# Kernel tuning notes

Hardware: AMD Instinct MI355X
Metric: run time of the kernel (lower is better)

Reference implementation:

```python
import jax, jax.numpy as jnp
import numpy as np

B, H, S, D = 2, 16, 2048, 128


def setup_inputs() -> dict:
    key = jax.random.key(0)
    kq, kk, kv = jax.random.split(key, 3)
    q = jax.random.normal(kq, (B, H, S, D), dtype=jnp.float32)
    k = jax.random.normal(kk, (B, H, S, D), dtype=jnp.float32)
    v = jax.random.normal(kv, (B, H, S, D), dtype=jnp.float32)
    scale = jnp.float32(1.0 / np.sqrt(D))
    return {"q": q, "k": k, "v": v, "scale": scale}


def reference(q, k, v, scale):
    # scores: [B, H, S, S]
    attn = jnp.einsum("bhqd,bhkd->bhqk", q, k) * scale
    attn = jnp.square(jax.nn.relu(attn))  # relu(x)^2 score function (no softmax)
    return jnp.einsum("bhqk,bhkd->bhqd", attn, v)
```

## Files before the change

kernel.cpp:

```cpp
#include <hip/hip_runtime.h>
#include <hip/hip_bf16.h>
#include <stdint.h>

#define S_LEN 2048
#define D_DIM 128
#define QT 128
#define KT 64
#define NT (S_LEN/KT)
#define TKT 32
#define TNT (S_LEN/TKT)

typedef float  f32x4  __attribute__((ext_vector_type(4)));
typedef float  f32x16 __attribute__((ext_vector_type(16)));
typedef short  bf16x8 __attribute__((ext_vector_type(8)));
typedef unsigned int uintx4 __attribute__((ext_vector_type(4)));

__device__ __forceinline__ short f2bf(float f) {
    return __builtin_bit_cast(short, __float2bfloat16(f));
}

__device__ __forceinline__ unsigned int pk2(float lo, float hi) {
    unsigned int d;
    asm("v_cvt_pk_bf16_f32 %0, %1, %2" : "=v"(d) : "v"(lo), "v"(hi));
    return d;
}

__device__ __forceinline__ void gload_lds16(const short* g, char* l) {
    __builtin_amdgcn_global_load_lds(
        (const __attribute__((address_space(1))) void*)g,
        (__attribute__((address_space(3))) void*)l,
        16, 0, 0);
}

__global__ __launch_bounds__(256)
void convert_k_kernel(const float* __restrict__ kin, short* __restrict__ kbf) {
    const size_t i = ((size_t)blockIdx.x * 256 + threadIdx.x) * 8;
    f32x4 a = *(const f32x4*)(kin + i);
    f32x4 c = *(const f32x4*)(kin + i + 4);
    bf16x8 t;
    t[0]=f2bf(a[0]); t[1]=f2bf(a[1]); t[2]=f2bf(a[2]); t[3]=f2bf(a[3]);
    t[4]=f2bf(c[0]); t[5]=f2bf(c[1]); t[6]=f2bf(c[2]); t[7]=f2bf(c[3]);
    *(bf16x8*)(kbf + i) = t;
}

__global__ __launch_bounds__(256)
void transpose_v_kernel(const float* __restrict__ vin, short* __restrict__ vt) {
    __shared__ short T[16 * 130];
    const int tid = threadIdx.x;
    const int blk = blockIdx.x;
    const int bh  = blk >> 3;
    const int d0  = (blk & 7) * 16;
    const float* vb = vin + (size_t)bh * S_LEN * D_DIM;
    short* vtb = vt + (size_t)bh * (size_t)D_DIM * S_LEN;
    const int c4 = tid & 3;
    const int rr = tid >> 2;
    const int dl = tid >> 4;
    const int kc = tid & 15;

    for (int kc0 = 0; kc0 < S_LEN; kc0 += 128) {
        #pragma unroll
        for (int h = 0; h < 2; ++h) {
            const int krow = kc0 + h*64 + rr;
            f32x4 a = *(const f32x4*)(vb + (size_t)krow * D_DIM + d0 + c4*4);
            #pragma unroll
            for (int j = 0; j < 4; ++j)
                T[(c4*4 + j)*130 + h*64 + rr] = f2bf(a[j]);
        }
        __syncthreads();
        int w0 = *(const int*)&T[dl*130 + kc*8 + 0];
        int w1 = *(const int*)&T[dl*130 + kc*8 + 2];
        int w2 = *(const int*)&T[dl*130 + kc*8 + 4];
        int w3 = *(const int*)&T[dl*130 + kc*8 + 6];
        int4 val = make_int4(w0, w1, w2, w3);
        *(int4*)(vtb + (size_t)(d0 + dl) * S_LEN + kc0 + kc*8) = val;
        __syncthreads();
    }
}

__global__ __launch_bounds__(256, 4)
void relu2_attn_main(const float* __restrict__ q,
                     const short* __restrict__ kbf,
                     const short* __restrict__ vtbf,
                     const float* __restrict__ scale_p,
                     float* __restrict__ out) {
    __shared__ __align__(16) char lds[32768];

    const int tid  = threadIdx.x;
    const int wave = tid >> 6;
    const int lane = tid & 63;
    const int l31  = lane & 31;
    const int hi   = lane >> 5;

    const int bid = blockIdx.x;
    const int bh  = bid & 31;
    const int qt  = bid >> 5;
    const int q0  = qt * QT;

    const float* qb = q    + (size_t)bh * S_LEN * D_DIM;
    const short* kb = kbf  + (size_t)bh * S_LEN * D_DIM;
    const short* vt = vtbf + (size_t)bh * (size_t)D_DIM * S_LEN;
    float*       ob = out  + (size_t)bh * S_LEN * D_DIM;

    const float scale = scale_p[0];

    const int RB = hi*512 + l31*16;

    int kOff[2], vOff[2];
    #pragma unroll
    for (int p = 0; p < 2; ++p) {
        const int s = (p*4 + wave)*64 + lane;
        kOff[p] = (s & 31)*128 + (s >> 6)*16 + ((s >> 5) & 1)*8;
        vOff[p] = ((s >> 7)*32 + (s & 31))*2048
                + ((s >> 6) & 1)*16 + ((s >> 5) & 1)*8;
    }

    bf16x8 qa[8];
    {
        const int qrow = q0 + wave*32 + l31;
        const float* qp = qb + (size_t)qrow * D_DIM + hi*8;
        #pragma unroll
        for (int dk = 0; dk < 8; ++dk) {
            f32x4 a = *(const f32x4*)(qp + dk*16);
            f32x4 c = *(const f32x4*)(qp + dk*16 + 4);
            bf16x8 t;
            t[0]=f2bf(a[0]*scale); t[1]=f2bf(a[1]*scale);
            t[2]=f2bf(a[2]*scale); t[3]=f2bf(a[3]*scale);
            t[4]=f2bf(c[0]*scale); t[5]=f2bf(c[1]*scale);
            t[6]=f2bf(c[2]*scale); t[7]=f2bf(c[3]*scale);
            qa[dk] = t;
        }
    }

    f32x16 oacc[4];
    #pragma unroll
    for (int df = 0; df < 4; ++df) oacc[df] = {};

#define STAGE(T, B) do {                                                      \
    const int k0_ = (T) * TKT;                                                \
    _Pragma("unroll")                                                         \
    for (int p_ = 0; p_ < 2; ++p_) {                                          \
        const int ch_ = p_*4 + wave;                                          \
        gload_lds16(kb + (size_t)k0_*128 + kOff[p_],                          \
                    lds + (B)*8192 + ch_*1024);                               \
        gload_lds16(vt + k0_ + vOff[p_],                                      \
                    lds + 16384 + (B)*8192 + ch_*1024);                       \
    }                                                                         \
} while (0)

#define TILE_COMPUTE(BUF) do {                                                \
    f32x16 s0 = {};                                                           \
    __builtin_amdgcn_s_setprio(1);                                            \
    _Pragma("unroll")                                                         \
    for (int dk = 0; dk < 8; ++dk) {                                          \
        bf16x8 a = *(const bf16x8*)(lds + (BUF)*8192 + RB + (dk<<10));        \
        s0 = __builtin_amdgcn_mfma_f32_32x32x16_bf16(a, qa[dk], s0, 0, 0, 0); \
    }                                                                         \
    __builtin_amdgcn_s_setprio(0);                                            \
              \
    bf16x8 pa[2];                                                             \
    {                                                                         \
        float pr[16];                                                         \
        _Pragma("unroll")                                                     \
        for (int r = 0; r < 16; ++r) {                                        \
            float m_ = fmaxf(s0[r], 0.f); pr[r] = m_ * m_;                    \
        }                                                                     \
        _Pragma("unroll")                                                     \
        for (int t2 = 0; t2 < 2; ++t2) {                                      \
            unsigned int X  = pk2(pr[8*t2+0], pr[8*t2+1]);                    \
            unsigned int Y  = pk2(pr[8*t2+4], pr[8*t2+5]);                    \
            unsigned int X2 = pk2(pr[8*t2+2], pr[8*t2+3]);                    \
            unsigned int Y2 = pk2(pr[8*t2+6], pr[8*t2+7]);                    \
            asm volatile("v_permlane32_swap_b32 %0, %1" : "+v"(X),  "+v"(Y)); \
            asm volatile("v_permlane32_swap_b32 %0, %1" : "+v"(X2), "+v"(Y2));\
            pa[t2] = __builtin_bit_cast(bf16x8, (uintx4){X, X2, Y, Y2});      \
        }                                                                     \
    }                                                                         \
    __builtin_amdgcn_s_setprio(1);                                            \
    _Pragma("unroll")                                                         \
    for (int s_ = 0; s_ < 2; ++s_) {                                          \
        _Pragma("unroll")                                                     \
        for (int df = 0; df < 4; ++df) {                                      \
            bf16x8 vf = *(const bf16x8*)(lds + 16384 + (BUF)*8192 + RB        \
                                         + (df<<11) + (s_<<10));              \
            oacc[df] = __builtin_amdgcn_mfma_f32_32x32x16_bf16(               \
                           pa[s_], vf, oacc[df], 0, 0, 0);                    \
        }                                                                     \
    }                                                                         \
    __builtin_amdgcn_s_setprio(0);                                            \
} while (0)

    STAGE(0, 0);

    #pragma unroll 1
    for (int p = 0; p < TNT/2; ++p) {
        __syncthreads();
        STAGE(2*p + 1, 1);
        TILE_COMPUTE(0);
        __syncthreads();
        STAGE((2*p + 2) & (TNT - 1), 0);
        TILE_COMPUTE(1);
    }

    #pragma unroll
    for (int df = 0; df < 4; ++df) {
        #pragma unroll
        for (int rg = 0; rg < 4; ++rg) {
            #pragma unroll
            for (int e = 0; e < 4; ++e) {
                const int row = q0 + wave*32 + rg*8 + hi*4 + e;
                ob[(size_t)row * D_DIM + df*32 + l31] = oacc[df][rg*4 + e];
            }
        }
    }
}

#define KS 136
#define VS 72
#define PS 72

__global__ __launch_bounds__(256, 2)
void relu2_attn_fallback(const float* __restrict__ q,
                         const float* __restrict__ k,
                         const float* __restrict__ v,
                         const float* __restrict__ scale_p,
                         float* __restrict__ out) {
    __shared__ short Klds[KT][KS];
    __shared__ short VTlds[D_DIM][VS];
    __shared__ short Plds[QT][PS];

    const int tid  = threadIdx.x;
    const int wave = tid >> 6;
    const int lane = tid & 63;
    const int l15  = lane & 15;
    const int lg   = lane >> 4;

    const int bid = blockIdx.x;
    const int bh  = bid & 31;
    const int qt  = bid >> 5;
    const int q0  = qt * QT;

    const float* qb = q + (size_t)bh * S_LEN * D_DIM;
    const float* kb = k + (size_t)bh * S_LEN * D_DIM;
    const float* vb = v + (size_t)bh * S_LEN * D_DIM;
    float*       ob = out + (size_t)bh * S_LEN * D_DIM;

    const float scale = scale_p[0];

    bf16x8 qa[2][4];
    {
        const int qrow = q0 + wave * 32;
        #pragma unroll
        for (int qf = 0; qf < 2; ++qf) {
            const float* qp = qb + (size_t)(qrow + qf*16 + l15) * D_DIM + lg * 8;
            #pragma unroll
            for (int dk = 0; dk < 4; ++dk) {
                f32x4 a = *(const f32x4*)(qp + dk*32);
                f32x4 c = *(const f32x4*)(qp + dk*32 + 4);
                bf16x8 t;
                t[0]=f2bf(a[0]*scale); t[1]=f2bf(a[1]*scale);
                t[2]=f2bf(a[2]*scale); t[3]=f2bf(a[3]*scale);
                t[4]=f2bf(c[0]*scale); t[5]=f2bf(c[1]*scale);
                t[6]=f2bf(c[2]*scale); t[7]=f2bf(c[3]*scale);
                qa[qf][dk] = t;
            }
        }
    }

    const int kr = tid >> 4;
    const int kc = tid & 15;
    const int vd = tid & 127;
    const int vh = (tid >> 7) * 32;

    f32x4 kreg[8];
    float vreg[32];

#define FLOAD_TILE(T) do {                                                    \
    const float* kp_ = kb + (size_t)((T) * KT) * D_DIM;                       \
    _Pragma("unroll")                                                         \
    for (int p = 0; p < 4; ++p) {                                             \
        const float* rp_ = kp_ + (size_t)(p*16 + kr) * D_DIM + kc*8;          \
        kreg[2*p]   = *(const f32x4*)rp_;                                     \
        kreg[2*p+1] = *(const f32x4*)(rp_ + 4);                               \
    }                                                                         \
    const float* vp_ = vb + (size_t)((T) * KT + vh) * D_DIM + vd;             \
    _Pragma("unroll")                                                         \
    for (int j = 0; j < 32; ++j) vreg[j] = vp_[(size_t)j * D_DIM];            \
} while (0)

#define FSTORE_TILE() do {                                                    \
    _Pragma("unroll")                                                         \
    for (int p = 0; p < 4; ++p) {                                             \
        f32x4 a_ = kreg[2*p], b_ = kreg[2*p+1];                               \
        bf16x8 w_;                                                            \
        w_[0]=f2bf(a_[0]); w_[1]=f2bf(a_[1]); w_[2]=f2bf(a_[2]); w_[3]=f2bf(a_[3]); \
        w_[4]=f2bf(b_[0]); w_[5]=f2bf(b_[1]); w_[6]=f2bf(b_[2]); w_[7]=f2bf(b_[3]); \
        *(bf16x8*)&Klds[p*16 + kr][kc*8] = w_;                                \
    }                                                                         \
    _Pragma("unroll")                                                         \
    for (int c = 0; c < 4; ++c) {                                             \
        bf16x8 w_;                                                            \
        w_[0]=f2bf(vreg[c*8+0]); w_[1]=f2bf(vreg[c*8+1]);                     \
        w_[2]=f2bf(vreg[c*8+2]); w_[3]=f2bf(vreg[c*8+3]);                     \
        w_[4]=f2bf(vreg[c*8+4]); w_[5]=f2bf(vreg[c*8+5]);                     \
        w_[6]=f2bf(vreg[c*8+6]); w_[7]=f2bf(vreg[c*8+7]);                     \
        *(bf16x8*)&VTlds[vd][vh + c*8] = w_;                                  \
    }                                                                         \
} while (0)

    f32x4 oacc[2][8];
    #pragma unroll
    for (int i = 0; i < 2; ++i)
        #pragma unroll
        for (int j = 0; j < 8; ++j)
            oacc[i][j] = f32x4{0.f, 0.f, 0.f, 0.f};

    FLOAD_TILE(0);

    for (int t = 0; t < NT; ++t) {
        FSTORE_TILE();
        __syncthreads();
        FLOAD_TILE((t + 1) & (NT - 1));

        f32x4 sacc[2][4];
        #pragma unroll
        for (int qf = 0; qf < 2; ++qf)
            #pragma unroll
            for (int kf = 0; kf < 4; ++kf)
                sacc[qf][kf] = f32x4{0.f, 0.f, 0.f, 0.f};

        #pragma unroll
        for (int dk = 0; dk < 4; ++dk) {
            #pragma unroll
            for (int kf = 0; kf < 4; ++kf) {
                bf16x8 bf = *(const bf16x8*)&Klds[kf*16 + l15][dk*32 + lg*8];
                #pragma unroll
                for (int qf = 0; qf < 2; ++qf)
                    sacc[qf][kf] = __builtin_amdgcn_mfma_f32_16x16x32_bf16(
                        qa[qf][dk], bf, sacc[qf][kf], 0, 0, 0);
            }
        }

        #pragma unroll
        for (int qf = 0; qf < 2; ++qf) {
            #pragma unroll
            for (int kf = 0; kf < 4; ++kf) {
                f32x4 sv = sacc[qf][kf];
                #pragma unroll
                for (int e = 0; e < 4; ++e) {
                    float r = fmaxf(sv[e], 0.f);
                    Plds[wave*32 + qf*16 + lg*4 + e][kf*16 + l15] = f2bf(r * r);
                }
            }
        }

        #pragma unroll
        for (int ks = 0; ks < 2; ++ks) {
            bf16x8 pa[2];
            #pragma unroll
            for (int qf = 0; qf < 2; ++qf)
                pa[qf] = *(const bf16x8*)&Plds[wave*32 + qf*16 + l15][ks*32 + lg*8];
            #pragma unroll
            for (int df = 0; df < 8; ++df) {
                bf16x8 vf = *(const bf16x8*)&VTlds[df*16 + l15][ks*32 + lg*8];
                #pragma unroll
                for (int qf = 0; qf < 2; ++qf)
                    oacc[qf][df] = __builtin_amdgcn_mfma_f32_16x16x32_bf16(
                        pa[qf], vf, oacc[qf][df], 0, 0, 0);
            }
        }
        __syncthreads();
    }

    #pragma unroll
    for (int qf = 0; qf < 2; ++qf) {
        #pragma unroll
        for (int df = 0; df < 8; ++df) {
            f32x4 o = oacc[qf][df];
            const int row = q0 + wave*32 + qf*16 + lg*4;
            float* op = ob + (size_t)row * D_DIM + df*16 + l15;
            op[0*D_DIM] = o[0];
            op[1*D_DIM] = o[1];
            op[2*D_DIM] = o[2];
            op[3*D_DIM] = o[3];
        }
    }
}

extern "C" void kernel_launch(void* const* d_in, const int* in_sizes, int n_in,
                              void* d_out, int out_size, void* d_ws, size_t ws_size,
                              hipStream_t stream) {
    const float* q = (const float*)d_in[0];
    const float* k = (const float*)d_in[1];
    const float* v = (const float*)d_in[2];
    const float* scale = (const float*)d_in[3];
    float* out = (float*)d_out;

    const size_t elems = (size_t)2 * 16 * S_LEN * D_DIM;
    const size_t need  = elems * 2 * 2;

    if (ws_size >= need) {
        short* kbf = (short*)d_ws;
        short* vtb = (short*)d_ws + elems;
        convert_k_kernel<<<dim3((int)(elems / (256 * 8))), dim3(256), 0, stream>>>(k, kbf);
        transpose_v_kernel<<<dim3(256), dim3(256), 0, stream>>>(v, vtb);
        relu2_attn_main<<<dim3(512), dim3(256), 0, stream>>>(q, kbf, vtb, scale, out);
    } else {
        relu2_attn_fallback<<<dim3(512), dim3(256), 0, stream>>>(q, k, v, scale, out);
    }
}
```

Baseline: 114.5 us.

## Triple-buffer K/V LDS tiles with partial vmcnt waits in main attention loop

```diff
diff --git a/kernel.cpp b/kernel.cpp
--- a/kernel.cpp
+++ b/kernel.cpp
@@ -77,13 +77,13 @@
     }
 }
 
-__global__ __launch_bounds__(256, 4)
+__global__ __launch_bounds__(256, 3)
 void relu2_attn_main(const float* __restrict__ q,
                      const short* __restrict__ kbf,
                      const short* __restrict__ vtbf,
                      const float* __restrict__ scale_p,
                      float* __restrict__ out) {
-    __shared__ __align__(16) char lds[32768];
+    __shared__ __align__(16) char lds[49152];
 
     const int tid  = threadIdx.x;
     const int wave = tid >> 6;
@@ -135,28 +135,27 @@
     #pragma unroll
     for (int df = 0; df < 4; ++df) oacc[df] = {};
 
-#define STAGE(T, B) do {                                                      \
+#define STAGE(T, CB) do {                                                     \
     const int k0_ = (T) * TKT;                                                \
     _Pragma("unroll")                                                         \
     for (int p_ = 0; p_ < 2; ++p_) {                                          \
         const int ch_ = p_*4 + wave;                                          \
         gload_lds16(kb + (size_t)k0_*128 + kOff[p_],                          \
-                    lds + (B)*8192 + ch_*1024);                               \
+                    lds + (CB) + ch_*1024);                                   \
         gload_lds16(vt + k0_ + vOff[p_],                                      \
-                    lds + 16384 + (B)*8192 + ch_*1024);                       \
+                    lds + (CB) + 8192 + ch_*1024);                            \
     }                                                                         \
 } while (0)
 
-#define TILE_COMPUTE(BUF) do {                                                \
+#define TILE_COMPUTE(CB) do {                                                 \
     f32x16 s0 = {};                                                           \
     __builtin_amdgcn_s_setprio(1);                                            \
     _Pragma("unroll")                                                         \
     for (int dk = 0; dk < 8; ++dk) {                                          \
-        bf16x8 a = *(const bf16x8*)(lds + (BUF)*8192 + RB + (dk<<10));        \
+        bf16x8 a = *(const bf16x8*)(lds + (CB) + RB + (dk<<10));              \
         s0 = __builtin_amdgcn_mfma_f32_32x32x16_bf16(a, qa[dk], s0, 0, 0, 0); \
     }                                                                         \
     __builtin_amdgcn_s_setprio(0);                                            \
-              \
     bf16x8 pa[2];                                                             \
     {                                                                         \
         float pr[16];                                                         \
@@ -180,7 +179,7 @@
     for (int s_ = 0; s_ < 2; ++s_) {                                          \
         _Pragma("unroll")                                                     \
         for (int df = 0; df < 4; ++df) {                                      \
-            bf16x8 vf = *(const bf16x8*)(lds + 16384 + (BUF)*8192 + RB        \
+            bf16x8 vf = *(const bf16x8*)(lds + (CB) + 8192 + RB               \
                                          + (df<<11) + (s_<<10));              \
             oacc[df] = __builtin_amdgcn_mfma_f32_32x32x16_bf16(               \
                            pa[s_], vf, oacc[df], 0, 0, 0);                    \
@@ -190,16 +189,21 @@
 } while (0)
 
     STAGE(0, 0);
+    STAGE(1, 16384);
+
+    int c0 = 0, c1 = 16384, c2 = 32768;
 
     #pragma unroll 1
-    for (int p = 0; p < TNT/2; ++p) {
-        __syncthreads();
-        STAGE(2*p + 1, 1);
-        TILE_COMPUTE(0);
-        __syncthreads();
-        STAGE((2*p + 2) & (TNT - 1), 0);
-        TILE_COMPUTE(1);
-    }
+    for (int t = 0; t < TNT; ++t) {
+        asm volatile("s_waitcnt vmcnt(4)" ::: "memory");
+        __builtin_amdgcn_s_barrier();
+        __builtin_amdgcn_sched_barrier(0);
+        STAGE((t + 2) & (TNT - 1), c2);
+        TILE_COMPUTE(c0);
+        const int tmp = c0; c0 = c1; c1 = c2; c2 = tmp;
+    }
+
+    asm volatile("s_waitcnt vmcnt(0)" ::: "memory");
 
     #pragma unroll
     for (int df = 0; df < 4; ++df) {
```

Result: faster. 101.7 us (-11.2%).
